# Kernel optimization log

Measured on AMD Instinct MI355X. Metric: run time of the kernel, lower is better.

The kernel has to match this reference:

```python
import jax, jax.numpy as jnp
import numpy as np

N = 100000   # nodes
E = 1600000  # edges
D = 128      # input feature dim
H = 128      # hidden dim
C = 40       # output classes


def _gcn_conv(x, W, b, src, dst, norm):
    # PyG GCNConv: h = x @ W; out_i = sum_j (d_i^-1/2 d_j^-1/2) h_j over in-edges,
    # including self-loops, then + bias. norm = deg^-1/2 with self-loop-augmented degree.
    h = x @ W                                    # [N, H]
    coef = norm[src] * norm[dst]                 # [E]
    agg = jax.ops.segment_sum(h[src] * coef[:, None], dst, num_segments=N)
    agg = agg + h * (norm * norm)[:, None]       # self-loop term
    return agg + b


def setup_inputs() -> dict:
    key = jax.random.key(0)
    ks = jax.random.split(key, 12)
    x = jax.random.normal(ks[0], (N, D), dtype=jnp.float32)
    edge_index = jax.random.randint(ks[1], (2, E), 0, N, dtype=jnp.int64)

    def lin(k, fan_in, fan_out):
        s = 1.0 / np.sqrt(fan_in)
        return jax.random.uniform(k, (fan_in, fan_out), jnp.float32, -s, s)

    return {
        "x": x,
        "edge_index": edge_index,
        "W1": lin(ks[2], D, H), "b1": jnp.zeros((H,), jnp.float32),
        "W2": lin(ks[3], H, H), "b2": jnp.zeros((H,), jnp.float32),
        "W3": lin(ks[4], H, H), "b3": jnp.zeros((H,), jnp.float32),
        "Wp1": lin(ks[5], H, H), "bp1": jnp.zeros((H,), jnp.float32),
        "Wp2": lin(ks[6], H, C), "bp2": jnp.zeros((C,), jnp.float32),
    }


def reference(x, edge_index, W1, b1, W2, b2, W3, b3, Wp1, bp1, Wp2, bp2):
    src, dst = edge_index[0], edge_index[1]
    # degree with self-loops (GCNConv adds self-loops by default)
    deg = jax.ops.segment_sum(jnp.ones((E,), jnp.float32), dst, num_segments=N) + 1.0
    norm = jax.lax.rsqrt(deg)                    # deg^-1/2

    h = x
    for W, b in ((W1, b1), (W2, b2), (W3, b3)):
        h = _gcn_conv(h, W, b, src, dst, norm)
        h = jax.nn.relu(h)
        # dropout is a no-op at inference / rate 0

    h = h @ Wp1 + bp1
    h = h @ Wp2 + bp2
    return jax.nn.log_softmax(h, axis=1)
```

## Files before the change

kernel.cpp:

```cpp
#include <hip/hip_runtime.h>
#include <hip/hip_bf16.h>
#include <math.h>


#define DH 128
#define NC 40
#define BN 256
#define MAXNB 512
#define CH 8192
#define ECAP 6144
#define SP 136

typedef __attribute__((ext_vector_type(8))) short bf16x8;
typedef __attribute__((ext_vector_type(4))) float f32x4;

__device__ __forceinline__ unsigned short f2bf(float f) {
    unsigned u = __float_as_uint(f);
    unsigned r = (u + 0x7fffu + ((u >> 16) & 1u)) >> 16;
    return (unsigned short)r;
}
__device__ __forceinline__ unsigned pack2(float lo, float hi) {
    return (unsigned)f2bf(lo) | ((unsigned)f2bf(hi) << 16);
}


__global__ __launch_bounds__(256) void bucket_hist(const int* __restrict__ dst, int E,
                                                   unsigned* __restrict__ bcnt) {
    __shared__ unsigned h[MAXNB];
    int tid = threadIdx.x;
    for (int i = tid; i < MAXNB; i += 256) h[i] = 0;
    __syncthreads();
    int e0 = blockIdx.x * CH;
    int e1 = min(e0 + CH, E);
    for (int i = e0 + tid; i < e1; i += 256)
        atomicAdd(&h[dst[i] >> 8], 1u);
    __syncthreads();
    for (int i = tid; i < MAXNB; i += 256)
        if (h[i]) atomicAdd(&bcnt[i], h[i]);
}

__global__ __launch_bounds__(256) void bucket_alloc(const unsigned* __restrict__ bcnt,
                                                    unsigned* __restrict__ bbase,
                                                    unsigned* __restrict__ bpos,
                                                    unsigned* __restrict__ cursor, int NB) {
    int i = blockIdx.x * 256 + threadIdx.x;
    if (i < NB) {
        unsigned c = bcnt[i];
        unsigned o = atomicAdd(cursor, c);
        bbase[i] = o;
        bpos[i] = o;
    }
}

__global__ __launch_bounds__(256) void bucket_scatter(const int* __restrict__ src,
                                                      const int* __restrict__ dst, int E,
                                                      unsigned* __restrict__ bpos,
                                                      unsigned* __restrict__ ebuf) {
    __shared__ unsigned hist[MAXNB];
    __shared__ unsigned lbase[MAXNB];
    __shared__ unsigned gbase[MAXNB];
    __shared__ unsigned cur[MAXNB];
    __shared__ unsigned sorted[CH];
    __shared__ unsigned short sbkt[CH];
    __shared__ unsigned total;

    int tid = threadIdx.x;
    int e0 = blockIdx.x * CH;
    int nE = min(CH, E - e0);

    for (int i = tid; i < MAXNB; i += 256) { hist[i] = 0; cur[i] = 0; }
    if (tid == 0) total = 0;
    __syncthreads();

    for (int i = tid; i < nE; i += 256)
        atomicAdd(&hist[dst[e0 + i] >> 8], 1u);
    __syncthreads();

    for (int i = tid; i < MAXNB; i += 256) {
        unsigned h = hist[i];
        lbase[i] = h ? atomicAdd(&total, h) : 0u;
        gbase[i] = h ? atomicAdd(&bpos[i], h) : 0u;
    }
    __syncthreads();

    for (int i = tid; i < nE; i += 256) {
        int s = src[e0 + i];
        int d = dst[e0 + i];
        unsigned b = (unsigned)d >> 8;
        unsigned r = atomicAdd(&cur[b], 1u);
        unsigned p = lbase[b] + r;
        sorted[p] = ((unsigned)s << 8) | ((unsigned)d & 255u);
        sbkt[p] = (unsigned short)b;
    }
    __syncthreads();

    for (int p = tid; p < nE; p += 256) {
        unsigned b = sbkt[p];
        ebuf[gbase[b] + (p - lbase[b])] = sorted[p];
    }
}

__global__ __launch_bounds__(256) void bucket_csr(const unsigned* __restrict__ ebuf,
                                                  const unsigned* __restrict__ bbase,
                                                  const unsigned* __restrict__ bcnt,
                                                  unsigned* __restrict__ off,
                                                  unsigned* __restrict__ cnt,
                                                  float* __restrict__ nrm,
                                                  int* __restrict__ csr, int N) {
    __shared__ unsigned h[BN];
    __shared__ unsigned nb[BN];
    __shared__ unsigned ncur[BN];
    __shared__ int lcsr[ECAP];
    __shared__ unsigned tot;

    int b = blockIdx.x;
    int tid = threadIdx.x;
    unsigned ebase = bbase[b];
    unsigned ecnt = bcnt[b];

    h[tid] = 0;
    if (tid == 0) tot = 0;
    __syncthreads();

    for (unsigned i = tid; i < ecnt; i += 256)
        atomicAdd(&h[ebuf[ebase + i] & 255u], 1u);
    __syncthreads();

    unsigned myh = h[tid];
    unsigned mybase = myh ? atomicAdd(&tot, myh) : 0u;
    nb[tid] = mybase;
    ncur[tid] = 0;
    int node = b * BN + tid;
    if (node < N) {
        off[node] = ebase + mybase;
        cnt[node] = myh;
        nrm[node] = rsqrtf((float)myh + 1.0f);
    }
    __syncthreads();

    if (ecnt <= ECAP) {
        for (unsigned i = tid; i < ecnt; i += 256) {
            unsigned v = ebuf[ebase + i];
            unsigned nl = v & 255u;
            unsigned r = atomicAdd(&ncur[nl], 1u);
            lcsr[nb[nl] + r] = (int)(v >> 8);
        }
        __syncthreads();
        for (unsigned i = tid; i < ecnt; i += 256)
            csr[ebase + i] = lcsr[i];
    } else {
        for (unsigned i = tid; i < ecnt; i += 256) {
            unsigned v = ebuf[ebase + i];
            unsigned nl = v & 255u;
            unsigned r = atomicAdd(&ncur[nl], 1u);
            csr[ebase + nb[nl] + r] = (int)(v >> 8);
        }
    }
}


__global__ __launch_bounds__(256) void prep_w(const float* __restrict__ W1,
                                              const float* __restrict__ W2,
                                              const float* __restrict__ W3,
                                              const float* __restrict__ Wp1,
                                              const float* __restrict__ bp1,
                                              const float* __restrict__ Wp2,
                                              const float* __restrict__ bp2,
                                              unsigned short* __restrict__ Wt,
                                              unsigned short* __restrict__ Wft,
                                              float* __restrict__ bfh) {
    int id = blockIdx.x * 256 + threadIdx.x;
    if (id < 3 * DH * DH) {
        int l = id >> 14, r = id & (DH * DH - 1);
        int k = r >> 7, n = r & 127;
        const float* W = (l == 0) ? W1 : (l == 1) ? W2 : W3;
        Wt[l * DH * DH + n * DH + k] = f2bf(W[k * DH + n]);
    } else if (id < 3 * DH * DH + 48 * DH) {
        int o = id - 3 * DH * DH;
        int c = o >> 7, k = o & 127;
        float acc = 0.f;
        if (c < NC)
            for (int j = 0; j < DH; ++j) acc += Wp1[k * DH + j] * Wp2[j * NC + c];
        Wft[c * DH + k] = f2bf(acc);
    } else if (id < 3 * DH * DH + 48 * DH + 48) {
        int c = id - 3 * DH * DH - 48 * DH;
        float acc = 0.f;
        if (c < NC) {
            acc = bp2[c];
            for (int j = 0; j < DH; ++j) acc += bp1[j] * Wp2[j * NC + c];
        }
        bfh[c] = acc;
    }
}


__global__ __launch_bounds__(256) void gemm_mfma_f32(const float* __restrict__ X,
                                                     const unsigned short* __restrict__ Wt,
                                                     const float* __restrict__ nrm,
                                                     unsigned short* __restrict__ outb,
                                                     int nrows) {
    const int tid = threadIdx.x;
    const int wave = tid >> 6;
    const int lane = tid & 63;
    const int m = lane & 15;
    const int quad = lane >> 4;
    const int rbase = blockIdx.x * 128 + wave * 32;

    union U8 { bf16x8 v; unsigned u[4]; };

    f32x4 acc[2][8];
#pragma unroll
    for (int rt = 0; rt < 2; ++rt)
#pragma unroll
        for (int ct = 0; ct < 8; ++ct) acc[rt][ct] = (f32x4){0.f, 0.f, 0.f, 0.f};

#pragma unroll
    for (int kt = 0; kt < 4; ++kt) {
        const int kof = kt * 32 + quad * 8;
        bf16x8 a[2], b[8];
#pragma unroll
        for (int rt = 0; rt < 2; ++rt) {
            int r = rbase + rt * 16 + m;
            r = (r < nrows) ? r : (nrows - 1);
            const float* p = X + (size_t)r * DH + kof;
            float4 u0 = *(const float4*)p;
            float4 u1 = *(const float4*)(p + 4);
            U8 t;
            t.u[0] = pack2(u0.x, u0.y);
            t.u[1] = pack2(u0.z, u0.w);
            t.u[2] = pack2(u1.x, u1.y);
            t.u[3] = pack2(u1.z, u1.w);
            a[rt] = t.v;
        }
#pragma unroll
        for (int ct = 0; ct < 8; ++ct)
            b[ct] = *(const bf16x8*)(Wt + (ct * 16 + m) * DH + kof);
#pragma unroll
        for (int rt = 0; rt < 2; ++rt)
#pragma unroll
            for (int ct = 0; ct < 8; ++ct)
                acc[rt][ct] = __builtin_amdgcn_mfma_f32_16x16x32_bf16(a[rt], b[ct], acc[rt][ct], 0, 0, 0);
    }

#pragma unroll
    for (int rt = 0; rt < 2; ++rt)
#pragma unroll
        for (int reg = 0; reg < 4; ++reg) {
            int r = rbase + rt * 16 + quad * 4 + reg;
            if (r < nrows) {
                float s = nrm[r];
#pragma unroll
                for (int ct = 0; ct < 8; ++ct)
                    outb[(size_t)r * DH + ct * 16 + m] = f2bf(acc[rt][ct][reg] * s);
            }
        }
}


__device__ __forceinline__ void bf8_add(float* acc, uint4 v) {
    acc[0] += __uint_as_float(v.x << 16);
    acc[1] += __uint_as_float(v.x & 0xffff0000u);
    acc[2] += __uint_as_float(v.y << 16);
    acc[3] += __uint_as_float(v.y & 0xffff0000u);
    acc[4] += __uint_as_float(v.z << 16);
    acc[5] += __uint_as_float(v.z & 0xffff0000u);
    acc[6] += __uint_as_float(v.w << 16);
    acc[7] += __uint_as_float(v.w & 0xffff0000u);
}

__device__ __forceinline__ void gather_phase(const uint4* __restrict__ Abf,
                                             const int* __restrict__ csr,
                                             const unsigned* __restrict__ off,
                                             const unsigned* __restrict__ cnt,
                                             const float* __restrict__ nrm,
                                             const float* __restrict__ bias,
                                             unsigned short (*sA)[SP], int N) {
    const int tid = threadIdx.x;
    const int g = tid >> 4;
    const int lane = tid & 15;
    const int node = blockIdx.x * 16 + g;
    if (node < N) {
        float acc[8];
        {
            uint4 v = Abf[(size_t)node * 16 + lane];
            acc[0] = __uint_as_float(v.x << 16);
            acc[1] = __uint_as_float(v.x & 0xffff0000u);
            acc[2] = __uint_as_float(v.y << 16);
            acc[3] = __uint_as_float(v.y & 0xffff0000u);
            acc[4] = __uint_as_float(v.z << 16);
            acc[5] = __uint_as_float(v.z & 0xffff0000u);
            acc[6] = __uint_as_float(v.w << 16);
            acc[7] = __uint_as_float(v.w & 0xffff0000u);
        }
        unsigned o = off[node];
        unsigned d = cnt[node];

        unsigned e = 0;
        for (; e + 4 <= d; e += 4) {
            int s0 = csr[o + e + 0];
            int s1 = csr[o + e + 1];
            int s2 = csr[o + e + 2];
            int s3 = csr[o + e + 3];
            uint4 v0 = Abf[(size_t)s0 * 16 + lane];
            uint4 v1 = Abf[(size_t)s1 * 16 + lane];
            uint4 v2 = Abf[(size_t)s2 * 16 + lane];
            uint4 v3 = Abf[(size_t)s3 * 16 + lane];
            bf8_add(acc, v0);
            bf8_add(acc, v1);
            bf8_add(acc, v2);
            bf8_add(acc, v3);
        }
        for (; e < d; ++e) {
            int s = csr[o + e];
            uint4 v = Abf[(size_t)s * 16 + lane];
            bf8_add(acc, v);
        }

        float nm = nrm[node];
        float4 b0 = *(const float4*)(bias + lane * 8);
        float4 b1 = *(const float4*)(bias + lane * 8 + 4);
        unsigned short* p = &sA[g][lane * 8];
        p[0] = f2bf(fmaxf(acc[0] * nm + b0.x, 0.f));
        p[1] = f2bf(fmaxf(acc[1] * nm + b0.y, 0.f));
        p[2] = f2bf(fmaxf(acc[2] * nm + b0.z, 0.f));
        p[3] = f2bf(fmaxf(acc[3] * nm + b0.w, 0.f));
        p[4] = f2bf(fmaxf(acc[4] * nm + b1.x, 0.f));
        p[5] = f2bf(fmaxf(acc[5] * nm + b1.y, 0.f));
        p[6] = f2bf(fmaxf(acc[6] * nm + b1.z, 0.f));
        p[7] = f2bf(fmaxf(acc[7] * nm + b1.w, 0.f));
    }
    __syncthreads();
}


__global__ __launch_bounds__(256) void agg_gemm(const uint4* __restrict__ Abf,
                                                const int* __restrict__ csr,
                                                const unsigned* __restrict__ off,
                                                const unsigned* __restrict__ cnt,
                                                const float* __restrict__ nrm,
                                                const float* __restrict__ bias,
                                                const unsigned short* __restrict__ Wt,
                                                unsigned short* __restrict__ outb, int N) {
    __shared__ unsigned short sA[16][SP];
    gather_phase(Abf, csr, off, cnt, nrm, bias, sA, N);

    const int tid = threadIdx.x;
    const int wave = tid >> 6;
    const int l64 = tid & 63;
    const int m = l64 & 15;
    const int quad = l64 >> 4;

    f32x4 acc[2];
    acc[0] = (f32x4){0.f, 0.f, 0.f, 0.f};
    acc[1] = (f32x4){0.f, 0.f, 0.f, 0.f};

#pragma unroll
    for (int kt = 0; kt < 4; ++kt) {
        const int kof = kt * 32 + quad * 8;
        bf16x8 a = *(const bf16x8*)&sA[m][kof];
#pragma unroll
        for (int c2 = 0; c2 < 2; ++c2) {
            const int ct = wave * 2 + c2;
            bf16x8 b = *(const bf16x8*)(Wt + (ct * 16 + m) * DH + kof);
            acc[c2] = __builtin_amdgcn_mfma_f32_16x16x32_bf16(a, b, acc[c2], 0, 0, 0);
        }
    }

#pragma unroll
    for (int reg = 0; reg < 4; ++reg) {
        int r = blockIdx.x * 16 + quad * 4 + reg;
        if (r < N) {
            float s = nrm[r];
#pragma unroll
            for (int c2 = 0; c2 < 2; ++c2)
                outb[(size_t)r * DH + (wave * 2 + c2) * 16 + m] = f2bf(acc[c2][reg] * s);
        }
    }
}


__global__ __launch_bounds__(256) void agg_head(const uint4* __restrict__ Abf,
                                                const int* __restrict__ csr,
                                                const unsigned* __restrict__ off,
                                                const unsigned* __restrict__ cnt,
                                                const float* __restrict__ nrm,
                                                const float* __restrict__ bias,
                                                const unsigned short* __restrict__ Wft,
                                                const float* __restrict__ bfh,
                                                float* __restrict__ out, int N) {
    __shared__ unsigned short sA[16][SP];
    gather_phase(Abf, csr, off, cnt, nrm, bias, sA, N);

    const int tid = threadIdx.x;
    if (tid >= 64) return;
    const int m = tid & 15;
    const int quad = tid >> 4;

    f32x4 acc[3];
#pragma unroll
    for (int ct = 0; ct < 3; ++ct) acc[ct] = (f32x4){0.f, 0.f, 0.f, 0.f};

#pragma unroll
    for (int kt = 0; kt < 4; ++kt) {
        const int kof = kt * 32 + quad * 8;
        bf16x8 a = *(const bf16x8*)&sA[m][kof];
#pragma unroll
        for (int ct = 0; ct < 3; ++ct) {
            bf16x8 b = *(const bf16x8*)(Wft + (ct * 16 + m) * DH + kof);
            acc[ct] = __builtin_amdgcn_mfma_f32_16x16x32_bf16(a, b, acc[ct], 0, 0, 0);
        }
    }

    float bias0 = bfh[m];
    float bias1 = bfh[16 + m];
    float bias2 = bfh[32 + m];

#pragma unroll
    for (int reg = 0; reg < 4; ++reg) {
        float v0 = acc[0][reg] + bias0;
        float v1 = acc[1][reg] + bias1;
        float v2 = (m < 8) ? (acc[2][reg] + bias2) : -1e30f;
        float mx = fmaxf(fmaxf(v0, v1), v2);
#pragma unroll
        for (int dlt = 1; dlt < 16; dlt <<= 1) mx = fmaxf(mx, __shfl_xor(mx, dlt));
        float s = __expf(v0 - mx) + __expf(v1 - mx) + ((m < 8) ? __expf(v2 - mx) : 0.f);
#pragma unroll
        for (int dlt = 1; dlt < 16; dlt <<= 1) s += __shfl_xor(s, dlt);
        float ls = mx + __logf(s);
        int r = blockIdx.x * 16 + quad * 4 + reg;
        if (r < N) {
            out[(size_t)r * NC + m] = v0 - ls;
            out[(size_t)r * NC + 16 + m] = v1 - ls;
            if (m < 8) out[(size_t)r * NC + 32 + m] = v2 - ls;
        }
    }
}


extern "C" void kernel_launch(void* const* d_in, const int* in_sizes, int n_in,
                              void* d_out, int out_size, void* d_ws, size_t ws_size,
                              hipStream_t stream) {
    const float* x   = (const float*)d_in[0];
    const int*   ei  = (const int*)d_in[1];
    const float* W1  = (const float*)d_in[2];
    const float* b1  = (const float*)d_in[3];
    const float* W2  = (const float*)d_in[4];
    const float* b2  = (const float*)d_in[5];
    const float* W3  = (const float*)d_in[6];
    const float* b3  = (const float*)d_in[7];
    const float* Wp1 = (const float*)d_in[8];
    const float* bp1 = (const float*)d_in[9];
    const float* Wp2 = (const float*)d_in[10];
    const float* bp2 = (const float*)d_in[11];
    float* out = (float*)d_out;

    const int N = in_sizes[0] / DH;
    const int E = in_sizes[1] / 2;
    const int* src = ei;
    const int* dst = ei + E;
    const int NB = (N + BN - 1) / BN;

    char* w = (char*)d_ws;
    unsigned short* Ab  = (unsigned short*)w; w += (size_t)N * DH * 2;
    unsigned short* Bb  = (unsigned short*)w; w += (size_t)N * DH * 2;
    int*      csr    = (int*)w;      w += (size_t)E * 4;
    unsigned* ebuf   = (unsigned*)w; w += (size_t)E * 4;
    unsigned* bcnt   = (unsigned*)w; w += MAXNB * 4;
    unsigned* cursor = (unsigned*)w; w += 16;
    unsigned* bbase  = (unsigned*)w; w += MAXNB * 4;
    unsigned* bpos   = (unsigned*)w; w += MAXNB * 4;
    unsigned* off    = (unsigned*)w; w += (size_t)N * 4;
    unsigned* cnt    = (unsigned*)w; w += (size_t)N * 4;
    float*    nrm    = (float*)w;    w += (size_t)N * 4;
    unsigned short* Wt  = (unsigned short*)w; w += 3 * DH * DH * 2;
    unsigned short* Wft = (unsigned short*)w; w += 48 * DH * 2;
    float*    bfh    = (float*)w;    w += 64 * 4;

    const int gC = (E + CH - 1) / CH;

    hipMemsetAsync(bcnt, 0, MAXNB * 4 + 16, stream);
    bucket_hist   <<<gC, 256, 0, stream>>>(dst, E, bcnt);
    bucket_alloc  <<<(NB + 255) / 256, 256, 0, stream>>>(bcnt, bbase, bpos, cursor, NB);
    bucket_scatter<<<gC, 256, 0, stream>>>(src, dst, E, bpos, ebuf);
    bucket_csr    <<<NB, 256, 0, stream>>>(ebuf, bbase, bcnt, off, cnt, nrm, csr, N);
    prep_w<<<(3 * DH * DH + 48 * DH + 48 + 255) / 256, 256, 0, stream>>>(
        W1, W2, W3, Wp1, bp1, Wp2, bp2, Wt, Wft, bfh);

    const int gG = (N + 127) / 128;
    const int gF = (N + 15) / 16;

    gemm_mfma_f32<<<gG, 256, 0, stream>>>(x, Wt, nrm, Ab, N);
    agg_gemm<<<gF, 256, 0, stream>>>((const uint4*)Ab, csr, off, cnt, nrm, b1,
                                     Wt + DH * DH, Bb, N);
    agg_gemm<<<gF, 256, 0, stream>>>((const uint4*)Bb, csr, off, cnt, nrm, b2,
                                     Wt + 2 * DH * DH, Ab, N);
    agg_head<<<gF, 256, 0, stream>>>((const uint4*)Ab, csr, off, cnt, nrm, b3,
                                     Wft, bfh, out, N);
}
```

Before: 418.0 us.

## Sort nodes by in-degree to balance gather work across blocks

Adds three small kernels that histogram node in-degrees, scan the histogram in descending order and scatter node ids into a permutation grouped by degree. The aggregation kernels then process nodes in that order, so each 16-node block handles nodes of similar degree, which reduces intra-block imbalance in the gather loop. In exchange it adds kernel launches, an extra indirection for every node read and output write, and output writes become scattered rather than contiguous.

```diff
diff --git a/kernel.cpp b/kernel.cpp
--- a/kernel.cpp
+++ b/kernel.cpp
@@ -155,6 +155,49 @@
             unsigned r = atomicAdd(&ncur[nl], 1u);
             csr[ebase + nb[nl] + r] = (int)(v >> 8);
         }
+    }
+}
+
+
+__global__ __launch_bounds__(256) void deg_hist(const unsigned* __restrict__ cnt, int N,
+                                                unsigned* __restrict__ dh) {
+    __shared__ unsigned h[256];
+    int t = threadIdx.x;
+    h[t] = 0;
+    __syncthreads();
+    int i = blockIdx.x * 256 + t;
+    if (i < N) atomicAdd(&h[min(cnt[i], 255u)], 1u);
+    __syncthreads();
+    if (h[t]) atomicAdd(&dh[t], h[t]);
+}
+
+__global__ __launch_bounds__(256) void deg_scan(const unsigned* __restrict__ dh,
+                                                unsigned* __restrict__ binpos) {
+    __shared__ unsigned s[256];
+    int t = threadIdx.x;
+    s[t] = dh[t];
+    __syncthreads();
+    unsigned sum = 0;
+    for (int d = t + 1; d < 256; ++d) sum += s[d];
+    binpos[t] = sum;
+}
+
+__global__ __launch_bounds__(256) void deg_scatter(const unsigned* __restrict__ cnt, int N,
+                                                   unsigned* __restrict__ binpos,
+                                                   int* __restrict__ perm) {
+    __shared__ unsigned h[256], base[256], cur[256];
+    int t = threadIdx.x;
+    h[t] = 0; cur[t] = 0;
+    __syncthreads();
+    int i = blockIdx.x * 256 + t;
+    unsigned d = 0;
+    if (i < N) { d = min(cnt[i], 255u); atomicAdd(&h[d], 1u); }
+    __syncthreads();
+    if (h[t]) base[t] = atomicAdd(&binpos[t], h[t]);
+    __syncthreads();
+    if (i < N) {
+        unsigned r = atomicAdd(&cur[d], 1u);
+        perm[base[d] + r] = i;
     }
 }
 
@@ -274,12 +317,14 @@
                                              const unsigned* __restrict__ cnt,
                                              const float* __restrict__ nrm,
                                              const float* __restrict__ bias,
+                                             const int* __restrict__ perm,
                                              unsigned short (*sA)[SP], int N) {
     const int tid = threadIdx.x;
     const int g = tid >> 4;
     const int lane = tid & 15;
-    const int node = blockIdx.x * 16 + g;
-    if (node < N) {
+    const int idx = blockIdx.x * 16 + g;
+    if (idx < N) {
+        const int node = perm[idx];
         float acc[8];
         {
             uint4 v = Abf[(size_t)node * 16 + lane];
@@ -339,10 +384,11 @@
                                                 const unsigned* __restrict__ cnt,
                                                 const float* __restrict__ nrm,
                                                 const float* __restrict__ bias,
+                                                const int* __restrict__ perm,
                                                 const unsigned short* __restrict__ Wt,
                                                 unsigned short* __restrict__ outb, int N) {
     __shared__ unsigned short sA[16][SP];
-    gather_phase(Abf, csr, off, cnt, nrm, bias, sA, N);
+    gather_phase(Abf, csr, off, cnt, nrm, bias, perm, sA, N);
 
     const int tid = threadIdx.x;
     const int wave = tid >> 6;
@@ -368,8 +414,9 @@
 
 #pragma unroll
     for (int reg = 0; reg < 4; ++reg) {
-        int r = blockIdx.x * 16 + quad * 4 + reg;
-        if (r < N) {
+        int idx = blockIdx.x * 16 + quad * 4 + reg;
+        if (idx < N) {
+            int r = perm[idx];
             float s = nrm[r];
 #pragma unroll
             for (int c2 = 0; c2 < 2; ++c2)
@@ -385,11 +432,12 @@
                                                 const unsigned* __restrict__ cnt,
                                                 const float* __restrict__ nrm,
                                                 const float* __restrict__ bias,
+                                                const int* __restrict__ perm,
                                                 const unsigned short* __restrict__ Wft,
                                                 const float* __restrict__ bfh,
                                                 float* __restrict__ out, int N) {
     __shared__ unsigned short sA[16][SP];
-    gather_phase(Abf, csr, off, cnt, nrm, bias, sA, N);
+    gather_phase(Abf, csr, off, cnt, nrm, bias, perm, sA, N);
 
     const int tid = threadIdx.x;
     if (tid >= 64) return;
@@ -427,8 +475,9 @@
 #pragma unroll
         for (int dlt = 1; dlt < 16; dlt <<= 1) s += __shfl_xor(s, dlt);
         float ls = mx + __logf(s);
-        int r = blockIdx.x * 16 + quad * 4 + reg;
-        if (r < N) {
+        int idx = blockIdx.x * 16 + quad * 4 + reg;
+        if (idx < N) {
+            int r = perm[idx];
             out[(size_t)r * NC + m] = v0 - ls;
             out[(size_t)r * NC + 16 + m] = v1 - ls;
             if (m < 8) out[(size_t)r * NC + 32 + m] = v2 - ls;
@@ -467,22 +516,29 @@
     unsigned* ebuf   = (unsigned*)w; w += (size_t)E * 4;
     unsigned* bcnt   = (unsigned*)w; w += MAXNB * 4;
     unsigned* cursor = (unsigned*)w; w += 16;
+    unsigned* dh     = (unsigned*)w; w += 256 * 4;
     unsigned* bbase  = (unsigned*)w; w += MAXNB * 4;
     unsigned* bpos   = (unsigned*)w; w += MAXNB * 4;
+    unsigned* binpos = (unsigned*)w; w += 256 * 4;
     unsigned* off    = (unsigned*)w; w += (size_t)N * 4;
     unsigned* cnt    = (unsigned*)w; w += (size_t)N * 4;
     float*    nrm    = (float*)w;    w += (size_t)N * 4;
+    int*      perm   = (int*)w;      w += (size_t)((N + 31) & ~31) * 4;
     unsigned short* Wt  = (unsigned short*)w; w += 3 * DH * DH * 2;
     unsigned short* Wft = (unsigned short*)w; w += 48 * DH * 2;
     float*    bfh    = (float*)w;    w += 64 * 4;
 
     const int gC = (E + CH - 1) / CH;
-
-    hipMemsetAsync(bcnt, 0, MAXNB * 4 + 16, stream);
+    const int gN = (N + 255) / 256;
+
+    hipMemsetAsync(bcnt, 0, MAXNB * 4 + 16 + 256 * 4, stream);
     bucket_hist   <<<gC, 256, 0, stream>>>(dst, E, bcnt);
     bucket_alloc  <<<(NB + 255) / 256, 256, 0, stream>>>(bcnt, bbase, bpos, cursor, NB);
     bucket_scatter<<<gC, 256, 0, stream>>>(src, dst, E, bpos, ebuf);
     bucket_csr    <<<NB, 256, 0, stream>>>(ebuf, bbase, bcnt, off, cnt, nrm, csr, N);
+    deg_hist      <<<gN, 256, 0, stream>>>(cnt, N, dh);
+    deg_scan      <<<1, 256, 0, stream>>>(dh, binpos);
+    deg_scatter   <<<gN, 256, 0, stream>>>(cnt, N, binpos, perm);
     prep_w<<<(3 * DH * DH + 48 * DH + 48 + 255) / 256, 256, 0, stream>>>(
         W1, W2, W3, Wp1, bp1, Wp2, bp2, Wt, Wft, bfh);
 
@@ -490,10 +546,10 @@
     const int gF = (N + 15) / 16;
 
     gemm_mfma_f32<<<gG, 256, 0, stream>>>(x, Wt, nrm, Ab, N);
-    agg_gemm<<<gF, 256, 0, stream>>>((const uint4*)Ab, csr, off, cnt, nrm, b1,
+    agg_gemm<<<gF, 256, 0, stream>>>((const uint4*)Ab, csr, off, cnt, nrm, b1, perm,
                                      Wt + DH * DH, Bb, N);
-    agg_gemm<<<gF, 256, 0, stream>>>((const uint4*)Bb, csr, off, cnt, nrm, b2,
+    agg_gemm<<<gF, 256, 0, stream>>>((const uint4*)Bb, csr, off, cnt, nrm, b2, perm,
                                      Wt + 2 * DH * DH, Ab, N);
-    agg_head<<<gF, 256, 0, stream>>>((const uint4*)Ab, csr, off, cnt, nrm, b3,
+    agg_head<<<gF, 256, 0, stream>>>((const uint4*)Ab, csr, off, cnt, nrm, b3, perm,
                                      Wft, bfh, out, N);
 }
```

Result: slower. 432.6 us (+3.5%).
